# Performance work log

Measured on AMD Instinct MI355X. Metric: run time of the kernel, lower is better.

## Reference

```python
import jax, jax.numpy as jnp
import numpy as np

B, C, M, T = 2, 512, 16, 128
H = 8
D = C // H  # 64, divisible by 4 for 2D RoPE
G = C // 4  # GroupNorm groups = 128
S = M * T


def group_norm(x, scale, bias, groups=G, eps=1e-5):
    b, c, m, t = x.shape
    xg = x.reshape(b, groups, c // groups, m, t)
    mu = xg.mean(axis=(2, 3, 4), keepdims=True)
    var = xg.var(axis=(2, 3, 4), keepdims=True)
    xn = ((xg - mu) * jax.lax.rsqrt(var + eps)).reshape(b, c, m, t)
    return xn * scale[None, :, None, None] + bias[None, :, None, None]


def dwsep_conv(x, dw, pw):
    # depthwise 3x3 (groups=C) then pointwise 1x1
    y = jax.lax.conv_general_dilated(
        x, dw, window_strides=(1, 1), padding='SAME',
        dimension_numbers=('NCHW', 'HWIO', 'NCHW'), feature_group_count=x.shape[1])
    return jnp.einsum('bcmt,cd->bdmt', y, pw)


def rope2d(x):
    # x: [B,H,M,T,D]; first D/2 dims rotated by freq index m, last D/2 by time index t
    d = x.shape[-1]
    dh = d // 2
    q = dh // 2
    inv = 1.0 / (10000.0 ** (jnp.arange(q, dtype=jnp.float32) / q))

    def rot(v, ang):
        h = v.shape[-1] // 2
        v1, v2 = v[..., :h], v[..., h:]
        c, s = jnp.cos(ang), jnp.sin(ang)
        return jnp.concatenate([v1 * c - v2 * s, v1 * s + v2 * c], axis=-1)

    ang_f = jnp.arange(x.shape[2], dtype=jnp.float32)[:, None] * inv  # [M,q]
    ang_t = jnp.arange(x.shape[3], dtype=jnp.float32)[:, None] * inv  # [T,q]
    xf = rot(x[..., :dh], ang_f[:, None, :])  # broadcast over T
    xt = rot(x[..., dh:], ang_t)
    return jnp.concatenate([xf, xt], axis=-1)


def setup_inputs() -> dict:
    key = jax.random.key(0)
    ks = jax.random.split(key, 14)
    s = 0.02
    return {
        'x': jax.random.normal(ks[0], (B, C, M, T), jnp.float32),
        'lengths': jax.random.randint(ks[1], (B,), T // 2, T + 1),
        'gn_scale': jnp.ones((C,), jnp.float32),
        'gn_bias': jnp.zeros((C,), jnp.float32),
        'dw_q': jax.random.normal(ks[2], (3, 3, 1, C), jnp.float32) * s,
        'dw_k': jax.random.normal(ks[3], (3, 3, 1, C), jnp.float32) * s,
        'dw_v': jax.random.normal(ks[4], (3, 3, 1, C), jnp.float32) * s,
        'pw_q': jax.random.normal(ks[5], (C, C), jnp.float32) * s,
        'pw_k': jax.random.normal(ks[6], (C, C), jnp.float32) * s,
        'pw_v': jax.random.normal(ks[7], (C, C), jnp.float32) * s,
        'attn_w': jax.random.normal(ks[8], (C, C), jnp.float32) * s,
        'attn_b': jnp.zeros((C,), jnp.float32),
        'out_w': jax.random.normal(ks[9], (C, C), jnp.float32) * s,
        'out_b': jnp.zeros((C,), jnp.float32),
    }


def reference(x, lengths, gn_scale, gn_bias, dw_q, dw_k, dw_v, pw_q, pw_k, pw_v,
              attn_w, attn_b, out_w, out_b):
    residual = x
    xn = group_norm(x, gn_scale, gn_bias)

    def to_heads(y):  # [B,C,M,T] -> [B,H,M,T,D]
        return y.reshape(B, H, D, M, T).transpose(0, 1, 3, 4, 2)

    q = rope2d(to_heads(dwsep_conv(xn, dw_q, pw_q)))
    k = rope2d(to_heads(dwsep_conv(xn, dw_k, pw_k)))
    v = to_heads(dwsep_conv(xn, dw_v, pw_v))

    q = q.reshape(B, H, S, D)
    k = k.reshape(B, H, S, D)
    v = v.reshape(B, H, S, D)

    scores = jnp.einsum('bhsd,bhkd->bhsk', q, k) / np.sqrt(D).astype(np.float32)
    valid_t = jnp.arange(T)[None, :] < lengths[:, None]        # [B,T]
    valid = jnp.tile(valid_t, (1, M))                          # [B,S], token idx = m*T + t
    scores = jnp.where(valid[:, None, None, :], scores, jnp.float32(-1e9))
    attn = jax.nn.softmax(scores, axis=-1)
    o = jnp.einsum('bhsk,bhkd->bhsd', attn, v)                 # [B,H,S,D]

    o = o.transpose(0, 2, 1, 3).reshape(B, S, C)
    o = o @ attn_w + attn_b                                    # block output proj
    o = o.reshape(B, M, T, C).transpose(0, 3, 1, 2)            # [B,C,M,T]
    out = jnp.einsum('bcmt,cd->bdmt', o, out_w) + out_b[None, :, None, None]
    return residual + out
```

## Files before the change

kernel.cpp:

```cpp
#include <hip/hip_runtime.h>
#include <math.h>

#define CCH 512
#define SSQ 2048
#define MTOT 4096

typedef __bf16 bf16;
typedef __bf16 bf16x8 __attribute__((ext_vector_type(8)));
typedef __bf16 bf16x4 __attribute__((ext_vector_type(4)));
typedef float  f32x4  __attribute__((ext_vector_type(4)));

#define AS1 __attribute__((address_space(1)))
#define AS3 __attribute__((address_space(3)))
__device__ __forceinline__ void glds16(const void* g, void* l) {
    __builtin_amdgcn_global_load_lds((const AS1 void*)g, (AS3 void*)l, 16, 0, 0);
}

__global__ __launch_bounds__(256) void gnw_kernel(const float* __restrict__ x,
        float* __restrict__ mu, float* __restrict__ rstd,
        const float* __restrict__ w0, const float* __restrict__ w1,
        const float* __restrict__ w2, const float* __restrict__ w3,
        const float* __restrict__ w4, bf16* __restrict__ wT,
        const float* __restrict__ attnb, const float* __restrict__ outb,
        float* __restrict__ bcv) {
    __shared__ float smem[64*65];
    int tid = threadIdx.x;
    if (blockIdx.x < 256) {
        float* s_sum = smem;
        float* s_sq  = smem + 256;
        int bg = blockIdx.x;
        long base = (long)bg * 8192;
        float sum = 0.f, sq = 0.f;
#pragma unroll
        for (int r = 0; r < 32; ++r) {
            float v = x[base + r*256 + tid];
            sum += v; sq += v*v;
        }
        s_sum[tid] = sum; s_sq[tid] = sq;
        __syncthreads();
        for (int off = 128; off > 0; off >>= 1) {
            if (tid < off) { s_sum[tid] += s_sum[tid+off]; s_sq[tid] += s_sq[tid+off]; }
            __syncthreads();
        }
        if (tid == 0) {
            float m = s_sum[0] * (1.f/8192.f);
            float v = s_sq[0]  * (1.f/8192.f) - m*m;
            mu[bg] = m;
            rstd[bg] = rsqrtf(v + 1e-5f);
        }
    } else if (blockIdx.x < 576) {
        int bid = blockIdx.x - 256;
        int z = bid >> 6, r2 = bid & 63;
        int k0 = (r2 >> 3)*64, n0 = (r2 & 7)*64;
        const float* srcs[5] = {w0, w1, w2, w3, w4};
        const float* W = srcs[z];
        bf16* D = wT + (long)z * (CCH*CCH);
        float (*t)[65] = (float(*)[65])smem;
        int cI = tid & 63, r4 = tid >> 6;
#pragma unroll
        for (int p = 0; p < 16; ++p) {
            int kr = p*4 + r4;
            t[kr][cI] = W[(long)(k0+kr)*CCH + n0 + cI];
        }
        __syncthreads();
#pragma unroll
        for (int p = 0; p < 16; ++p) {
            int nr = p*4 + r4;
            D[(long)(n0+nr)*CCH + k0 + cI] = (bf16)t[cI][nr];
        }
    } else if (blockIdx.x < 578) {
        int n = (blockIdx.x - 576)*256 + tid;
        float a = outb[n];
        for (int j = 0; j < 512; ++j)
            a = fmaf(attnb[j], w4[(long)j*CCH + n], a);
        bcv[n] = a;
    } else {
        bf16* wAc = wT + (long)5*CCH*CCH;
        int base = (blockIdx.x - 578)*4096 + tid;
#pragma unroll
        for (int p = 0; p < 16; ++p)
            wAc[base + p*256] = (bf16)w3[base + p*256];
    }
}

__global__ void tn_kernel(const float* __restrict__ x, const float* __restrict__ mu,
                          const float* __restrict__ rstd, const float* __restrict__ gsc,
                          const float* __restrict__ gbs, bf16* __restrict__ xnT) {
    __shared__ float t[64][65];
    int s0 = blockIdx.x*64, c0 = blockIdx.y*64, b = blockIdx.z;
    int tid = threadIdx.x;
    int cI = tid & 63, r4 = tid >> 6;
#pragma unroll
    for (int p = 0; p < 16; ++p) {
        int cr = p*4 + r4;
        t[cr][cI] = x[((long)(b*CCH + c0 + cr))*SSQ + s0 + cI];
    }
    __syncthreads();
#pragma unroll
    for (int p = 0; p < 16; ++p) {
        int sr = p*4 + r4;
        int c = c0 + cI;
        int g = b*128 + (c >> 2);
        float v = (t[cI][sr] - mu[g]) * rstd[g] * gsc[c] + gbs[c];
        xnT[((long)(b*SSQ + s0 + sr))*CCH + c] = (bf16)v;
    }
}

__global__ __launch_bounds__(256) void dw3_kernel(const bf16* __restrict__ xnT,
        const float* __restrict__ dwq, const float* __restrict__ dwk,
        const float* __restrict__ dwv,
        bf16* __restrict__ yq, bf16* __restrict__ yk, bf16* __restrict__ yv) {
    int tid = threadIdx.x;
    int cc = (tid & 63) * 8;
    int s  = blockIdx.x*4 + (tid >> 6);
    int sl = s & (SSQ-1);
    int b  = s >> 11;
    int m = sl >> 7, t = sl & 127;
    float aq[8] = {}, ak[8] = {}, av[8] = {};
#pragma unroll
    for (int di = 0; di < 3; ++di) {
        int m2 = m + di - 1;
        if ((unsigned)m2 >= 16u) continue;
#pragma unroll
        for (int dj = 0; dj < 3; ++dj) {
            int t2 = t + dj - 1;
            if ((unsigned)t2 >= 128u) continue;
            bf16x8 xv = *(const bf16x8*)(xnT + ((long)(b*SSQ + m2*128 + t2))*CCH + cc);
            int wi = (di*3 + dj)*CCH + cc;
#pragma unroll
            for (int i = 0; i < 8; ++i) {
                float xf = (float)xv[i];
                aq[i] += xf * dwq[wi+i];
                ak[i] += xf * dwk[wi+i];
                av[i] += xf * dwv[wi+i];
            }
        }
    }
    bf16x8 oq, ok, ov;
#pragma unroll
    for (int i = 0; i < 8; ++i) { oq[i] = (bf16)aq[i]; ok[i] = (bf16)ak[i]; ov[i] = (bf16)av[i]; }
    long o = (long)s*CCH + cc;
    *(bf16x8*)(yq + o) = oq;
    *(bf16x8*)(yk + o) = ok;
    *(bf16x8*)(yv + o) = ov;
}

template<int NFR>
__device__ __forceinline__ void gemm_core128(const bf16* __restrict__ A,
        const bf16* __restrict__ Wt, int m0, int n0,
        bf16* As, bf16* Bs, f32x4 (&acc)[4][NFR]) {
    int tid = threadIdx.x, lane = tid & 63, wid = tid >> 6;
    int sw = wid & 1, nw = wid >> 1;
    int col = lane & 15, quad = lane >> 4;
    const char* gA[4]; char* ldsA[4];
#pragma unroll
    for (int p = 0; p < 4; ++p) {
        int ci = tid + p*256;
        int row = ci >> 3;
        int c = (ci & 7) ^ (row & 7);
        gA[p] = (const char*)A + ((long)(m0+row)*CCH + c*8)*2;
        ldsA[p] = (char*)As + ci*16;
    }
    const char* gB[NFR]; char* ldsB[NFR];
#pragma unroll
    for (int p = 0; p < NFR; ++p) {
        int ci = tid + p*256;
        int row = ci >> 3;
        int c = (ci & 7) ^ (row & 7);
        gB[p] = (const char*)Wt + ((long)(n0+row)*CCH + c*8)*2;
        ldsB[p] = (char*)Bs + ci*16;
    }
    int rowA = sw*64 + col;
    int rowB = nw*(NFR*16) + col;
    for (int k0 = 0; k0 < CCH; k0 += 64) {
        __syncthreads();
#pragma unroll
        for (int p = 0; p < 4; ++p)   glds16(gA[p] + k0*2, ldsA[p]);
#pragma unroll
        for (int p = 0; p < NFR; ++p) glds16(gB[p] + k0*2, ldsB[p]);
        __syncthreads();
        bf16x8 af[4][2], bfr[NFR][2];
#pragma unroll
        for (int mt = 0; mt < 4; ++mt) {
            int r = rowA + mt*16;
#pragma unroll
            for (int ks = 0; ks < 2; ++ks) {
                int c = (ks*4 + quad) ^ (r & 7);
                af[mt][ks] = *(const bf16x8*)((char*)As + r*128 + c*16);
            }
        }
#pragma unroll
        for (int nt = 0; nt < NFR; ++nt) {
            int r = rowB + nt*16;
#pragma unroll
            for (int ks = 0; ks < 2; ++ks) {
                int c = (ks*4 + quad) ^ (r & 7);
                bfr[nt][ks] = *(const bf16x8*)((char*)Bs + r*128 + c*16);
            }
        }
#pragma unroll
        for (int ks = 0; ks < 2; ++ks)
#pragma unroll
            for (int mt = 0; mt < 4; ++mt)
#pragma unroll
                for (int nt = 0; nt < NFR; ++nt)
                    acc[mt][nt] = __builtin_amdgcn_mfma_f32_16x16x32_bf16(
                        af[mt][ks], bfr[nt][ks], acc[mt][nt], 0,0,0);
    }
}

__global__ __launch_bounds__(256) void gemm_qkv(const bf16* __restrict__ Abase,
        bf16* __restrict__ wT, bf16* __restrict__ qout,
        bf16* __restrict__ kout, bf16* __restrict__ vout) {
    __shared__ bf16 As[128*64];
    __shared__ bf16 Bs[64*64];
    int z = blockIdx.z;
    if (z == 3 && blockIdx.x >= 4) return;
    int m0 = blockIdx.x*128, n0 = blockIdx.y*64;
    const bf16* Aop = (z < 3) ? Abase + (long)z*MTOT*CCH : wT + (long)4*CCH*CCH;
    const bf16* Wop = (z < 3) ? wT + (long)z*CCH*CCH   : wT + (long)5*CCH*CCH;
    f32x4 acc[4][2] = {};
    gemm_core128<2>(Aop, Wop, m0, n0, As, Bs, acc);
    int tid = threadIdx.x, lane = tid & 63, wid = tid >> 6;
    int sw = wid & 1, nw = wid >> 1;
    int col = lane & 15, quad = lane >> 4;
    int nb = n0 + nw*32, mb = m0 + sw*64;
    if (z == 3) {
        bf16* wCt = wT + (long)6*CCH*CCH;
#pragma unroll
        for (int nt = 0; nt < 2; ++nt) {
            int n = nb + nt*16 + col;
#pragma unroll
            for (int mt = 0; mt < 4; ++mt)
#pragma unroll
                for (int r = 0; r < 4; ++r)
                    wCt[(long)(mb + mt*16 + quad*4 + r)*CCH + n] = (bf16)acc[mt][nt][r];
        }
    } else if (z < 2) {
        bf16* outp = z ? kout : qout;
        const float sc = z ? 1.0f : 0.125f;
        float invf = __expf(-(float)col * 0.5756462732485114f);
        bool tHalf = (nb & 32) != 0;
#pragma unroll
        for (int mt = 0; mt < 4; ++mt)
#pragma unroll
            for (int r = 0; r < 4; ++r) {
                int row = mb + mt*16 + quad*4 + r;
                int sl = row & (SSQ-1);
                float pos = tHalf ? (float)(sl & 127) : (float)(sl >> 7);
                float ang = pos * invf;
                float sn, cs;
                __sincosf(ang, &sn, &cs);
                float x1 = acc[mt][0][r], x2 = acc[mt][1][r];
                outp[(long)row*CCH + nb + col]      = (bf16)((x1*cs - x2*sn)*sc);
                outp[(long)row*CCH + nb + 16 + col] = (bf16)((x1*sn + x2*cs)*sc);
            }
    } else {
#pragma unroll
        for (int mt = 0; mt < 4; ++mt)
#pragma unroll
            for (int nt = 0; nt < 2; ++nt) {
                int n = nb + nt*16 + col;
                int row0 = mb + mt*16 + quad*4;
                int bq = row0 >> 11, sl0 = row0 & (SSQ-1);
                bf16x4 pk;
#pragma unroll
                for (int r = 0; r < 4; ++r) pk[r] = (bf16)acc[mt][nt][r];
                *(bf16x4*)(vout + ((long)(bq*CCH + n))*SSQ + sl0) = pk;
            }
    }
}

__global__ __launch_bounds__(256) void gemm_out(const bf16* __restrict__ A,
        const bf16* __restrict__ Wt, const float* __restrict__ bias,
        const float* __restrict__ resid, float* __restrict__ outp) {
    __shared__ bf16 As[128*64];
    __shared__ bf16 Bs[64*64];
    int m0 = blockIdx.x*128, n0 = blockIdx.y*64;
    f32x4 acc[4][2] = {};
    gemm_core128<2>(A, Wt, m0, n0, As, Bs, acc);
    int tid = threadIdx.x, lane = tid & 63, wid = tid >> 6;
    int sw = wid & 1, nw = wid >> 1;
    int col = lane & 15, quad = lane >> 4;
    int nb = n0 + nw*32, mb = m0 + sw*64;
#pragma unroll
    for (int mt = 0; mt < 4; ++mt)
#pragma unroll
        for (int nt = 0; nt < 2; ++nt) {
            int n = nb + nt*16 + col;
            float bv = bias[n];
            int row0 = mb + mt*16 + quad*4;
            int b = row0 >> 11, sl0 = row0 & (SSQ-1);
            long off = ((long)(b*CCH + n))*SSQ + sl0;
            float4 rr = *(const float4*)(resid + off);
            float4 o4;
            o4.x = acc[mt][nt][0] + bv + rr.x;
            o4.y = acc[mt][nt][1] + bv + rr.y;
            o4.z = acc[mt][nt][2] + bv + rr.z;
            o4.w = acc[mt][nt][3] + bv + rr.w;
            *(float4*)(outp + off) = o4;
        }
}

__global__ __launch_bounds__(512) void attn_kernel(
        const bf16* __restrict__ qb, const bf16* __restrict__ kb,
        const bf16* __restrict__ vb, const int* __restrict__ lengths,
        bf16* __restrict__ o) {
    __shared__ char KVs[2][32768];
    __shared__ bf16 Ps[8][32*72];
    __shared__ float Lm[4][2][16];
    int bid = blockIdx.x;
    int bh = bid & 15, qtb = bid >> 4;
    int b = bh >> 3, h = bh & 7;
    int tid = threadIdx.x, wid = tid >> 6, lane = tid & 63;
    int col = lane & 15, quad = lane >> 4;
    int qh = wid & 3, kh = wid >> 2;
    int q0 = qtb*128 + qh*32;
    int lenb = lengths[b];

    const char* gp[4]; long gstep[4]; int ldsoff[4];
#pragma unroll
    for (int p = 0; p < 4; ++p) {
        int idx = tid + p*512;
        int half = idx >> 10;
        int rem2 = idx & 1023;
        int isV = rem2 >> 9;
        int rem = rem2 & 511;
        int r = rem >> 3;
        int csrc = (rem & 7) ^ (r & 7);
        if (!isV) { gp[p] = (const char*)kb + ((long)(b*SSQ + half*1024 + r))*1024 + h*128 + csrc*16; gstep[p] = 65536; }
        else      { gp[p] = (const char*)vb + ((long)(b*CCH + h*64 + r))*4096 + half*2048 + csrc*16;  gstep[p] = 128; }
        ldsoff[p] = idx*16;
    }

    f32x4 mb[4];
#pragma unroll
    for (int sub = 0; sub < 4; ++sub)
#pragma unroll
        for (int r = 0; r < 4; ++r)
            mb[sub][r] = (64 + sub*16 + quad*4 + r < lenb) ? 0.f : -10000.f;

    const bf16* qp = qb + (long)(b*SSQ)*CCH + h*64;
    bf16x8 qf[2][2];
#pragma unroll
    for (int qt2 = 0; qt2 < 2; ++qt2)
#pragma unroll
        for (int dc = 0; dc < 2; ++dc)
            qf[qt2][dc] = *(const bf16x8*)(qp + (long)(q0 + qt2*16 + col)*CCH + dc*32 + quad*8);

    f32x4 of[2][4] = {};
    float ls0 = 0.f, ls1 = 0.f;
    bf16* pw = Ps[wid];
    int cswz = col & 7;

#pragma unroll
    for (int p = 0; p < 4; ++p) glds16(gp[p], KVs[0] + ldsoff[p]);
    __syncthreads();

    for (int t = 0; t < 16; ++t) {
        if (t < 15) {
#pragma unroll
            for (int p = 0; p < 4; ++p)
                glds16(gp[p] + (long)(t+1)*gstep[p], KVs[(t+1) & 1] + ldsoff[p]);
        }
        const bf16* K = (const bf16*)(KVs[t & 1] + kh*16384);
        const bf16* V = (const bf16*)(KVs[t & 1] + kh*16384 + 8192);
        bool masked = (t & 1) != 0;
        f32x4 sc[4][2];
#pragma unroll
        for (int sub = 0; sub < 4; ++sub)
#pragma unroll
            for (int qt2 = 0; qt2 < 2; ++qt2)
                sc[sub][qt2] = masked ? mb[sub] : (f32x4){0.f,0.f,0.f,0.f};
#pragma unroll
        for (int sub = 0; sub < 4; ++sub)
#pragma unroll
            for (int dc = 0; dc < 2; ++dc) {
                bf16x8 kf = *(const bf16x8*)((const char*)K + (sub*16 + col)*128 + (((dc*4+quad) ^ cswz))*16);
#pragma unroll
                for (int qt2 = 0; qt2 < 2; ++qt2)
                    sc[sub][qt2] = __builtin_amdgcn_mfma_f32_16x16x32_bf16(
                        kf, qf[qt2][dc], sc[sub][qt2], 0,0,0);
            }
#pragma unroll
        for (int sub = 0; sub < 4; ++sub)
#pragma unroll
            for (int qt2 = 0; qt2 < 2; ++qt2) {
                bf16x4 pk;
#pragma unroll
                for (int r = 0; r < 4; ++r) {
                    float p = __expf(sc[sub][qt2][r]);
                    if (qt2) ls1 += p; else ls0 += p;
                    pk[r] = (bf16)p;
                }
                *(bf16x4*)(pw + (qt2*16 + col)*72 + sub*16 + quad*4) = pk;
            }
#pragma unroll
        for (int ks = 0; ks < 2; ++ks) {
            bf16x8 pf0 = *(const bf16x8*)(pw + col*72 + ks*32 + quad*8);
            bf16x8 pf1 = *(const bf16x8*)(pw + (16 + col)*72 + ks*32 + quad*8);
#pragma unroll
            for (int dt = 0; dt < 4; ++dt) {
                bf16x8 vf = *(const bf16x8*)((const char*)V + (dt*16 + col)*128 + (((ks*4+quad) ^ cswz))*16);
                of[0][dt] = __builtin_amdgcn_mfma_f32_16x16x32_bf16(pf0, vf, of[0][dt], 0,0,0);
                of[1][dt] = __builtin_amdgcn_mfma_f32_16x16x32_bf16(pf1, vf, of[1][dt], 0,0,0);
            }
        }
        __syncthreads();
    }

    ls0 += __shfl_xor(ls0, 16); ls0 += __shfl_xor(ls0, 32);
    ls1 += __shfl_xor(ls1, 16); ls1 += __shfl_xor(ls1, 32);

    float* Om = (float*)KVs;
    if (kh == 1) {
#pragma unroll
        for (int qt2 = 0; qt2 < 2; ++qt2)
#pragma unroll
            for (int dt = 0; dt < 4; ++dt)
#pragma unroll
                for (int r = 0; r < 4; ++r)
                    Om[(qh*32 + qt2*16 + quad*4 + r)*64 + dt*16 + col] = of[qt2][dt][r];
        if (quad == 0) { Lm[qh][0][col] = ls0; Lm[qh][1][col] = ls1; }
    }
    __syncthreads();
    if (kh == 0) {
        float i0 = 1.f / (ls0 + Lm[qh][0][col]);
        float i1 = 1.f / (ls1 + Lm[qh][1][col]);
        bf16* ob = o + (long)(b*SSQ + q0)*CCH + h*64;
#pragma unroll
        for (int qt2 = 0; qt2 < 2; ++qt2) {
            float inv = qt2 ? i1 : i0;
            float ir[4];
#pragma unroll
            for (int r = 0; r < 4; ++r) ir[r] = __shfl(inv, quad*4 + r);
#pragma unroll
            for (int dt = 0; dt < 4; ++dt)
#pragma unroll
                for (int r = 0; r < 4; ++r) {
                    float v = of[qt2][dt][r] + Om[(qh*32 + qt2*16 + quad*4 + r)*64 + dt*16 + col];
                    ob[(long)(qt2*16 + quad*4 + r)*CCH + dt*16 + col] = (bf16)(v * ir[r]);
                }
        }
    }
}

extern "C" void kernel_launch(void* const* d_in, const int* in_sizes, int n_in,
                              void* d_out, int out_size, void* d_ws, size_t ws_size,
                              hipStream_t stream) {
    const float* x        = (const float*)d_in[0];
    const int*   lengths  = (const int*)  d_in[1];
    const float* gn_scale = (const float*)d_in[2];
    const float* gn_bias  = (const float*)d_in[3];
    const float* dw_q     = (const float*)d_in[4];
    const float* dw_k     = (const float*)d_in[5];
    const float* dw_v     = (const float*)d_in[6];
    const float* pw_q     = (const float*)d_in[7];
    const float* pw_k     = (const float*)d_in[8];
    const float* pw_v     = (const float*)d_in[9];
    const float* attn_w   = (const float*)d_in[10];
    const float* attn_b   = (const float*)d_in[11];
    const float* out_w    = (const float*)d_in[12];
    const float* out_b    = (const float*)d_in[13];
    float* out = (float*)d_out;

    char* w = (char*)d_ws;
    float* mu   = (float*)w;
    float* rstd = (float*)(w + 1024);
    float* bcv  = (float*)(w + 2048);
    bf16* wT    = (bf16*)(w + 4096);
    bf16* wCt = wT + (long)6*CCH*CCH;
    bf16* xnT  = (bf16*)(w + 0x00400000);
    bf16* yT   = (bf16*)(w + 0x00800000);
    bf16* qbf  = (bf16*)(w + 0x01400000);
    bf16* kbf  = (bf16*)(w + 0x01800000);
    bf16* vbf  = (bf16*)(w + 0x01C00000);
    bf16* obf  = (bf16*)(w + 0x02000000);

    gnw_kernel<<<642, 256, 0, stream>>>(x, mu, rstd, pw_q, pw_k, pw_v, attn_w, out_w,
                                        wT, attn_b, out_b, bcv);
    tn_kernel<<<dim3(32,8,2), 256, 0, stream>>>(x, mu, rstd, gn_scale, gn_bias, xnT);
    dw3_kernel<<<MTOT/4, 256, 0, stream>>>(xnT, dw_q, dw_k, dw_v,
                                           yT, yT + (long)MTOT*CCH, yT + (long)2*MTOT*CCH);

    gemm_qkv<<<dim3(MTOT/128, CCH/64, 4), 256, 0, stream>>>(yT, wT, qbf, kbf, vbf);

    attn_kernel<<<256, 512, 0, stream>>>(qbf, kbf, vbf, lengths, obf);

    gemm_out<<<dim3(MTOT/128, CCH/64), 256, 0, stream>>>(obf, wCt, bcv, x, out);
}
```

Baseline: 168.1 us.

## Keep softmax probabilities in registers and permute V reads to skip LDS round-trip

The attention kernel no longer writes exp'd scores to a per-wave LDS buffer and reads them back as MFMA A-operands. Instead it packs the probabilities straight from the score accumulators into bf16x8 fragments and permutes the key index inside each 32-wide k-slice, fetching matching V rows with two 4-element LDS reads. The change also folds the mask into a per-lane threshold, precomputes swizzled LDS offsets, sets MFMA priority and adds a launch-bounds occupancy hint. This trades LDS traffic and shared-memory footprint for split V loads and possible register pressure from the occupancy hint.

```diff
diff --git a/kernel.cpp b/kernel.cpp
--- a/kernel.cpp
+++ b/kernel.cpp
@@ -71,6 +71,7 @@
     } else if (blockIdx.x < 578) {
         int n = (blockIdx.x - 576)*256 + tid;
         float a = outb[n];
+#pragma unroll 16
         for (int j = 0; j < 512; ++j)
             a = fmaf(attnb[j], w4[(long)j*CCH + n], a);
         bcv[n] = a;
@@ -302,12 +303,11 @@
         }
 }
 
-__global__ __launch_bounds__(512) void attn_kernel(
+__global__ __launch_bounds__(512, 4) void attn_kernel(
         const bf16* __restrict__ qb, const bf16* __restrict__ kb,
         const bf16* __restrict__ vb, const int* __restrict__ lengths,
         bf16* __restrict__ o) {
     __shared__ char KVs[2][32768];
-    __shared__ bf16 Ps[8][32*72];
     __shared__ float Lm[4][2][16];
     int bid = blockIdx.x;
     int bh = bid & 15, qtb = bid >> 4;
@@ -316,29 +316,22 @@
     int col = lane & 15, quad = lane >> 4;
     int qh = wid & 3, kh = wid >> 2;
     int q0 = qtb*128 + qh*32;
-    int lenb = lengths[b];
-
-    const char* gp[4]; long gstep[4]; int ldsoff[4];
+    int thr = lengths[b] - 64 - quad*4;
+
+    const char* gp[4]; int ldsoff[4];
 #pragma unroll
     for (int p = 0; p < 4; ++p) {
         int idx = tid + p*512;
-        int half = idx >> 10;
-        int rem2 = idx & 1023;
-        int isV = rem2 >> 9;
-        int rem = rem2 & 511;
+        int half = p >> 1;
+        int rem = idx & 511;
         int r = rem >> 3;
         int csrc = (rem & 7) ^ (r & 7);
-        if (!isV) { gp[p] = (const char*)kb + ((long)(b*SSQ + half*1024 + r))*1024 + h*128 + csrc*16; gstep[p] = 65536; }
-        else      { gp[p] = (const char*)vb + ((long)(b*CCH + h*64 + r))*4096 + half*2048 + csrc*16;  gstep[p] = 128; }
+        if ((p & 1) == 0)
+            gp[p] = (const char*)kb + ((long)(b*SSQ + half*1024 + r))*1024 + h*128 + csrc*16;
+        else
+            gp[p] = (const char*)vb + ((long)(b*CCH + h*64 + r))*4096 + half*2048 + csrc*16;
         ldsoff[p] = idx*16;
     }
-
-    f32x4 mb[4];
-#pragma unroll
-    for (int sub = 0; sub < 4; ++sub)
-#pragma unroll
-        for (int r = 0; r < 4; ++r)
-            mb[sub][r] = (64 + sub*16 + quad*4 + r < lenb) ? 0.f : -10000.f;
 
     const bf16* qp = qb + (long)(b*SSQ)*CCH + h*64;
     bf16x8 qf[2][2];
@@ -350,8 +343,14 @@
 
     f32x4 of[2][4] = {};
     float ls0 = 0.f, ls1 = 0.f;
-    bf16* pw = Ps[wid];
     int cswz = col & 7;
+    int kbase0 = col*128 + ((0*4 + quad) ^ cswz)*16;
+    int kbase1 = col*128 + ((1*4 + quad) ^ cswz)*16;
+    int qh2 = quad >> 1, qlo = (quad & 1)*8;
+    int vlo0 = col*128 + ((0 + qh2) ^ cswz)*16 + qlo;
+    int vhi0 = col*128 + ((4 + qh2) ^ cswz)*16 + qlo;
+    int vlo1 = col*128 + ((2 + qh2) ^ cswz)*16 + qlo;
+    int vhi1 = col*128 + ((6 + qh2) ^ cswz)*16 + qlo;
 
 #pragma unroll
     for (int p = 0; p < 4; ++p) glds16(gp[p], KVs[0] + ldsoff[p]);
@@ -360,51 +359,68 @@
     for (int t = 0; t < 16; ++t) {
         if (t < 15) {
 #pragma unroll
-            for (int p = 0; p < 4; ++p)
-                glds16(gp[p] + (long)(t+1)*gstep[p], KVs[(t+1) & 1] + ldsoff[p]);
-        }
-        const bf16* K = (const bf16*)(KVs[t & 1] + kh*16384);
-        const bf16* V = (const bf16*)(KVs[t & 1] + kh*16384 + 8192);
-        bool masked = (t & 1) != 0;
+            for (int p = 0; p < 4; ++p) {
+                long step = (p & 1) ? 128L : 65536L;
+                glds16(gp[p] + (long)(t+1)*step, KVs[(t+1) & 1] + ldsoff[p]);
+            }
+        }
+        const char* K = KVs[t & 1] + kh*16384;
+        const char* V = K + 8192;
         f32x4 sc[4][2];
-#pragma unroll
-        for (int sub = 0; sub < 4; ++sub)
-#pragma unroll
-            for (int qt2 = 0; qt2 < 2; ++qt2)
-                sc[sub][qt2] = masked ? mb[sub] : (f32x4){0.f,0.f,0.f,0.f};
-#pragma unroll
-        for (int sub = 0; sub < 4; ++sub)
-#pragma unroll
-            for (int dc = 0; dc < 2; ++dc) {
-                bf16x8 kf = *(const bf16x8*)((const char*)K + (sub*16 + col)*128 + (((dc*4+quad) ^ cswz))*16);
-#pragma unroll
-                for (int qt2 = 0; qt2 < 2; ++qt2)
-                    sc[sub][qt2] = __builtin_amdgcn_mfma_f32_16x16x32_bf16(
-                        kf, qf[qt2][dc], sc[sub][qt2], 0,0,0);
-            }
-#pragma unroll
-        for (int sub = 0; sub < 4; ++sub)
+        if (t & 1) {
+#pragma unroll
+            for (int sub = 0; sub < 4; ++sub) {
+                f32x4 m;
+#pragma unroll
+                for (int r = 0; r < 4; ++r) m[r] = (sub*16 + r < thr) ? 0.f : -10000.f;
+                sc[sub][0] = m; sc[sub][1] = m;
+            }
+        } else {
+#pragma unroll
+            for (int sub = 0; sub < 4; ++sub) {
+                sc[sub][0] = (f32x4){0.f,0.f,0.f,0.f};
+                sc[sub][1] = (f32x4){0.f,0.f,0.f,0.f};
+            }
+        }
+        __builtin_amdgcn_s_setprio(1);
+#pragma unroll
+        for (int sub = 0; sub < 4; ++sub) {
+            bf16x8 kf0 = *(const bf16x8*)(K + sub*2048 + kbase0);
+            bf16x8 kf1 = *(const bf16x8*)(K + sub*2048 + kbase1);
+            sc[sub][0] = __builtin_amdgcn_mfma_f32_16x16x32_bf16(kf0, qf[0][0], sc[sub][0], 0,0,0);
+            sc[sub][1] = __builtin_amdgcn_mfma_f32_16x16x32_bf16(kf0, qf[1][0], sc[sub][1], 0,0,0);
+            sc[sub][0] = __builtin_amdgcn_mfma_f32_16x16x32_bf16(kf1, qf[0][1], sc[sub][0], 0,0,0);
+            sc[sub][1] = __builtin_amdgcn_mfma_f32_16x16x32_bf16(kf1, qf[1][1], sc[sub][1], 0,0,0);
+        }
+        __builtin_amdgcn_s_setprio(0);
+#pragma unroll
+        for (int ks = 0; ks < 2; ++ks) {
+            bf16x8 pf[2];
 #pragma unroll
             for (int qt2 = 0; qt2 < 2; ++qt2) {
-                bf16x4 pk;
+                float s = 0.f;
 #pragma unroll
                 for (int r = 0; r < 4; ++r) {
-                    float p = __expf(sc[sub][qt2][r]);
-                    if (qt2) ls1 += p; else ls0 += p;
-                    pk[r] = (bf16)p;
+                    float e0 = __expf(sc[ks][qt2][r]);
+                    float e1 = __expf(sc[ks+2][qt2][r]);
+                    pf[qt2][r]     = (bf16)e0;
+                    pf[qt2][4 + r] = (bf16)e1;
+                    s += e0 + e1;
                 }
-                *(bf16x4*)(pw + (qt2*16 + col)*72 + sub*16 + quad*4) = pk;
-            }
-#pragma unroll
-        for (int ks = 0; ks < 2; ++ks) {
-            bf16x8 pf0 = *(const bf16x8*)(pw + col*72 + ks*32 + quad*8);
-            bf16x8 pf1 = *(const bf16x8*)(pw + (16 + col)*72 + ks*32 + quad*8);
+                if (qt2) ls1 += s; else ls0 += s;
+            }
+            int vlo = ks ? vlo1 : vlo0;
+            int vhi = ks ? vhi1 : vhi0;
+            __builtin_amdgcn_s_setprio(1);
 #pragma unroll
             for (int dt = 0; dt < 4; ++dt) {
-                bf16x8 vf = *(const bf16x8*)((const char*)V + (dt*16 + col)*128 + (((ks*4+quad) ^ cswz))*16);
-                of[0][dt] = __builtin_amdgcn_mfma_f32_16x16x32_bf16(pf0, vf, of[0][dt], 0,0,0);
-                of[1][dt] = __builtin_amdgcn_mfma_f32_16x16x32_bf16(pf1, vf, of[1][dt], 0,0,0);
-            }
+                bf16x4 lo = *(const bf16x4*)(V + dt*2048 + vlo);
+                bf16x4 hi = *(const bf16x4*)(V + dt*2048 + vhi);
+                bf16x8 vf = {lo[0],lo[1],lo[2],lo[3],hi[0],hi[1],hi[2],hi[3]};
+                of[0][dt] = __builtin_amdgcn_mfma_f32_16x16x32_bf16(pf[0], vf, of[0][dt], 0,0,0);
+                of[1][dt] = __builtin_amdgcn_mfma_f32_16x16x32_bf16(pf[1], vf, of[1][dt], 0,0,0);
+            }
+            __builtin_amdgcn_s_setprio(0);
         }
         __syncthreads();
     }
```

After: 176.9 us. 1.05x slower.
